# Kernel tuning notes

Measured on AMD Instinct MI355X. Metric: run time of the kernel, lower is better.

Reference implementation:

```python
import jax, jax.numpy as jnp
import numpy as np

N, T1, T2 = 150000, 30000, 8192
E1, E2 = 400000, 160000
F_IN, F_HID, F_OUT = 512, 256, 20


def setup_inputs() -> dict:
    key = jax.random.key(0)
    ks = jax.random.split(key, 10)
    return {
        "x": jax.random.normal(ks[0], (N, F_IN), dtype=jnp.float32),
        "src1": jax.random.randint(ks[1], (E1,), 0, N, dtype=jnp.int32),
        "dst1": jax.random.randint(ks[2], (E1,), 0, T1, dtype=jnp.int32),
        "src2": jax.random.randint(ks[3], (E2,), 0, T1, dtype=jnp.int32),
        "dst2": jax.random.randint(ks[4], (E2,), 0, T2, dtype=jnp.int32),
        "Wl1": jax.random.normal(ks[5], (F_HID, F_IN), dtype=jnp.float32) * 0.05,
        "bl1": jnp.zeros((F_HID,), dtype=jnp.float32),
        "Wr1": jax.random.normal(ks[6], (F_HID, F_IN), dtype=jnp.float32) * 0.05,
        "Wl2": jax.random.normal(ks[7], (F_OUT, F_HID), dtype=jnp.float32) * 0.05,
        "bl2": jnp.zeros((F_OUT,), dtype=jnp.float32),
        "Wr2": jax.random.normal(ks[8], (F_OUT, F_HID), dtype=jnp.float32) * 0.05,
    }


def _sage_conv(x_src, x_tgt, src, dst, num_tgt, Wl, bl, Wr):
    # PyG SAGEConv (mean aggr, root_weight=True, bias on lin_l):
    # out = lin_l(mean_{j in N(i)} x_src[j]) + lin_r(x_tgt[i])
    msg = x_src[src]                                                  # [E, F]
    agg = jax.ops.segment_sum(msg, dst, num_segments=num_tgt)        # [T, F]
    cnt = jax.ops.segment_sum(jnp.ones((src.shape[0],), x_src.dtype), dst,
                              num_segments=num_tgt)                  # [T]
    mean = agg / jnp.maximum(cnt, 1.0)[:, None]
    return mean @ Wl.T + bl + x_tgt @ Wr.T


def reference(x, src1, dst1, src2, dst2, Wl1, bl1, Wr1, Wl2, bl2, Wr2):
    # Layer 1: [N, F_IN] -> [T1, F_HID], relu (eval mode: no dropout)
    h = _sage_conv(x, x[:T1], src1, dst1, T1, Wl1, bl1, Wr1)
    h = jax.nn.relu(h)
    # Layer 2: [T1, F_HID] -> [T2, F_OUT]
    out = _sage_conv(h, h[:T2], src2, dst2, T2, Wl2, bl2, Wr2)
    return jax.nn.log_softmax(out, axis=-1)
```

## Files before the change

kernel.cpp:

```cpp
#include <hip/hip_runtime.h>
#include <math.h>

constexpr int T1N  = 30000;
constexpr int T2N  = 8192;
constexpr int FIN  = 512;
constexpr int FHID = 256;
constexpr int FOUT = 20;

typedef short bf16x8 __attribute__((ext_vector_type(8)));
typedef float f32x4  __attribute__((ext_vector_type(4)));

__device__ __forceinline__ short f2bf(float f) {
    unsigned u = __float_as_uint(f);
    u += 0x7fff + ((u >> 16) & 1);
    return (short)(u >> 16);
}
__device__ __forceinline__ float bf2f(short s) {
    return __uint_as_float(((unsigned)(unsigned short)s) << 16);
}

__device__ __forceinline__ void gload16(const void* g, void* l) {
    __builtin_amdgcn_global_load_lds(
        (const __attribute__((address_space(1))) void*)g,
        (__attribute__((address_space(3))) void*)l, 16, 0, 0);
}

__global__ void count_kernel(const int* __restrict__ dst, int* __restrict__ cnt, int E) {
    int i = blockIdx.x * blockDim.x + threadIdx.x;
    int stride = gridDim.x * blockDim.x;
    for (; i < E; i += stride) atomicAdd(&cnt[dst[i]], 1);
}

__global__ __launch_bounds__(1024) void scan_kernel(const int* __restrict__ cnt,
        int* __restrict__ rs, int* __restrict__ cur, int T) {
    __shared__ int wsum[16];
    int tid = threadIdx.x;
    int lane = tid & 63, wid = tid >> 6;
    int carry = 0;
    for (int base = 0; base < T; base += 4096) {
        int i = base + tid * 4;
        int4 v = make_int4(0, 0, 0, 0);
        if (i + 3 < T) v = *(const int4*)(cnt + i);
        else {
            if (i     < T) v.x = cnt[i];
            if (i + 1 < T) v.y = cnt[i + 1];
            if (i + 2 < T) v.z = cnt[i + 2];
            if (i + 3 < T) v.w = cnt[i + 3];
        }
        int tsum = v.x + v.y + v.z + v.w;
        int s = tsum;
        #pragma unroll
        for (int off = 1; off < 64; off <<= 1) {
            int t = __shfl_up(s, off, 64);
            if (lane >= off) s += t;
        }
        if (lane == 63) wsum[wid] = s;
        __syncthreads();
        if (wid == 0) {
            int w = (lane < 16) ? wsum[lane] : 0;
            #pragma unroll
            for (int off = 1; off < 16; off <<= 1) {
                int t = __shfl_up(w, off, 64);
                if (lane >= off) w += t;
            }
            if (lane < 16) wsum[lane] = w;
        }
        __syncthreads();
        int e0 = s - tsum + (wid > 0 ? wsum[wid - 1] : 0) + carry;
        int e1 = e0 + v.x, e2 = e1 + v.y, e3 = e2 + v.z;
        if (i + 3 < T) {
            *(int4*)(rs + i)  = make_int4(e0, e1, e2, e3);
            *(int4*)(cur + i) = make_int4(e0, e1, e2, e3);
        } else {
            if (i     < T) { rs[i]     = e0; cur[i]     = e0; }
            if (i + 1 < T) { rs[i + 1] = e1; cur[i + 1] = e1; }
            if (i + 2 < T) { rs[i + 2] = e2; cur[i + 2] = e2; }
        }
        int total = wsum[15];
        __syncthreads();
        carry += total;
    }
    if (tid == 0) rs[T] = carry;
}

__global__ void scatter_kernel(const int* __restrict__ src, const int* __restrict__ dst,
        int* __restrict__ cur, int* __restrict__ ss, int E) {
    int i = blockIdx.x * blockDim.x + threadIdx.x;
    int stride = gridDim.x * blockDim.x;
    for (; i < E; i += stride) {
        int d = dst[i];
        int pos = atomicAdd(&cur[d], 1);
        ss[pos] = src[i];
    }
}

__global__ void convert_x_full(const float* __restrict__ x, short* __restrict__ xbf, long n8) {
    long i = ((long)blockIdx.x * blockDim.x + threadIdx.x);
    if (i >= n8) return;
    const float* p = x + i * 8;
    float4 v0 = *(const float4*)p;
    float4 v1 = *(const float4*)(p + 4);
    bf16x8 o;
    o[0] = f2bf(v0.x); o[1] = f2bf(v0.y); o[2] = f2bf(v0.z); o[3] = f2bf(v0.w);
    o[4] = f2bf(v1.x); o[5] = f2bf(v1.y); o[6] = f2bf(v1.z); o[7] = f2bf(v1.w);
    *(bf16x8*)(xbf + i * 8) = o;
}

__global__ void convert_w_kernel(const float* __restrict__ Wl, const float* __restrict__ Wr,
        short* __restrict__ Wcat) {
    int i = (blockIdx.x * blockDim.x + threadIdx.x) * 8;
    if (i >= FHID * 1024) return;
    int n = i >> 10;
    int k = i & 1023;
    const float* sp = (k < 512) ? (Wl + (size_t)n * FIN + k) : (Wr + (size_t)n * FIN + (k - 512));
    float4 v0 = *(const float4*)sp;
    float4 v1 = *(const float4*)(sp + 4);
    bf16x8 o;
    o[0] = f2bf(v0.x); o[1] = f2bf(v0.y); o[2] = f2bf(v0.z); o[3] = f2bf(v0.w);
    o[4] = f2bf(v1.x); o[5] = f2bf(v1.y); o[6] = f2bf(v1.z); o[7] = f2bf(v1.w);
    *(bf16x8*)(Wcat + (size_t)n * 1024 + k) = o;
}

__global__ void agg1_kernel(const short* __restrict__ xbf, const int* __restrict__ ss,
        const int* __restrict__ rs, short* __restrict__ meanbf, int T) {
    int gw = (int)((blockIdx.x * (size_t)blockDim.x + threadIdx.x) >> 6);
    int lane = threadIdx.x & 63;
    if (gw >= T) return;
    int j0 = rs[gw], j1 = rs[gw + 1];
    float a[8] = {};
    for (int j = j0; j < j1; ++j) {
        int s = ss[j];
        bf16x8 v = *(const bf16x8*)(xbf + (size_t)s * FIN + lane * 8);
        #pragma unroll
        for (int q = 0; q < 8; ++q) a[q] += bf2f(v[q]);
    }
    int d = j1 - j0;
    float inv = 1.0f / (float)(d > 1 ? d : 1);
    bf16x8 o;
    #pragma unroll
    for (int q = 0; q < 8; ++q) o[q] = f2bf(a[q] * inv);
    *(bf16x8*)(meanbf + (size_t)gw * FIN + lane * 8) = o;
}

__global__ void agg2_kernel(const float* __restrict__ feat, const int* __restrict__ ss,
        const int* __restrict__ rs, float* __restrict__ mean, int T) {
    int gw = (int)((blockIdx.x * (size_t)blockDim.x + threadIdx.x) >> 6);
    int lane = threadIdx.x & 63;
    if (gw >= T) return;
    int j0 = rs[gw], j1 = rs[gw + 1];
    float4 a = make_float4(0.f, 0.f, 0.f, 0.f);
    for (int j = j0; j < j1; ++j) {
        int s = ss[j];
        float4 v = *(const float4*)(feat + (size_t)s * FHID + lane * 4);
        a.x += v.x; a.y += v.y; a.z += v.z; a.w += v.w;
    }
    int d = j1 - j0;
    float inv = 1.0f / (float)(d > 1 ? d : 1);
    *(float4*)(mean + (size_t)gw * FHID + lane * 4) =
        make_float4(a.x * inv, a.y * inv, a.z * inv, a.w * inv);
}

__global__ __launch_bounds__(256, 2) void gemm1_mfma(
        const short* __restrict__ Am, const short* __restrict__ Ax,
        const short* __restrict__ W, const float* __restrict__ bias,
        float* __restrict__ h) {
    __shared__ short As[2][128 * 32];
    __shared__ short Bs[2][128 * 32];
    int tid = threadIdx.x;
    int wid = tid >> 6, lane = tid & 63;
    int brow = blockIdx.x * 128, bcol = blockIdx.y * 128;
    int wr = (wid >> 1) * 64, wc = (wid & 1) * 64;

    f32x4 acc[4][4] = {};
    int kgrp = lane >> 4;
    int r16 = lane & 15;

    auto stage = [&](int buf, int kt) {
        const short* Abase = (kt < 512) ? Am : Ax;
        int ko = kt & 511;
        #pragma unroll
        for (int c2 = 0; c2 < 2; ++c2) {
            int q = wid + c2 * 4;
            int c = q * 64 + lane;
            int row = c >> 2;
            int rx = (row ^ (row >> 2)) & 3;
            int sl = (c & 3) ^ rx;
            int gr = brow + row; if (gr > T1N - 1) gr = T1N - 1;
            gload16(Abase + (size_t)gr * 512 + ko + sl * 8, (char*)As[buf] + q * 1024);
            gload16(W + (size_t)(bcol + row) * 1024 + kt + sl * 8, (char*)Bs[buf] + q * 1024);
        }
    };

    stage(0, 0);
    __syncthreads();

    int cur = 0;
    for (int kt = 0; kt < 1024; kt += 32) {
        if (kt + 32 < 1024) stage(cur ^ 1, kt + 32);

        bf16x8 af[4], bfr[4];
        #pragma unroll
        for (int m = 0; m < 4; ++m) {
            int row = wr + m * 16 + r16;
            int sl = kgrp ^ ((row ^ (row >> 2)) & 3);
            af[m] = *(const bf16x8*)((const char*)As[cur] + row * 64 + sl * 16);
        }
        #pragma unroll
        for (int n = 0; n < 4; ++n) {
            int row = wc + n * 16 + r16;
            int sl = kgrp ^ ((row ^ (row >> 2)) & 3);
            bfr[n] = *(const bf16x8*)((const char*)Bs[cur] + row * 64 + sl * 16);
        }
        #pragma unroll
        for (int m = 0; m < 4; ++m)
            #pragma unroll
            for (int n = 0; n < 4; ++n)
                acc[m][n] = __builtin_amdgcn_mfma_f32_16x16x32_bf16(
                        af[m], bfr[n], acc[m][n], 0, 0, 0);

        __syncthreads();
        cur ^= 1;
    }

    int g4 = lane >> 4;
    #pragma unroll
    for (int n = 0; n < 4; ++n) {
        int col = bcol + wc + n * 16 + r16;
        float bv = bias[col];
        #pragma unroll
        for (int m = 0; m < 4; ++m) {
            #pragma unroll
            for (int r = 0; r < 4; ++r) {
                int row = brow + wr + m * 16 + g4 * 4 + r;
                if (row < T1N) {
                    float v = acc[m][n][r] + bv;
                    h[(size_t)row * FHID + col] = v > 0.f ? v : 0.f;
                }
            }
        }
    }
}

__global__ __launch_bounds__(256) void gemm2_lsm_kernel(const float* __restrict__ mean2,
        const float* __restrict__ h, const float* __restrict__ Wl,
        const float* __restrict__ Wr, const float* __restrict__ bias,
        float* __restrict__ out) {
    __shared__ float Wls[FOUT * FHID];
    __shared__ float Wrs[FOUT * FHID];
    int tid = threadIdx.x;
    for (int i = tid; i < FOUT * FHID / 4; i += 256) {
        ((float4*)Wls)[i] = ((const float4*)Wl)[i];
        ((float4*)Wrs)[i] = ((const float4*)Wr)[i];
    }
    __syncthreads();

    int row = blockIdx.x * 4 + (tid >> 6);
    int lane = tid & 63;
    if (row >= T2N) return;

    float acc[FOUT];
    #pragma unroll
    for (int o = 0; o < FOUT; ++o) acc[o] = 0.f;

    const float* mrow = mean2 + (size_t)row * FHID;
    const float* hrow = h + (size_t)row * FHID;
    #pragma unroll
    for (int kk = 0; kk < 4; ++kk) {
        int k = lane + kk * 64;
        float m = mrow[k];
        float hr = hrow[k];
        #pragma unroll
        for (int o = 0; o < FOUT; ++o)
            acc[o] = fmaf(m, Wls[o * FHID + k], fmaf(hr, Wrs[o * FHID + k], acc[o]));
    }
    #pragma unroll
    for (int o = 0; o < FOUT; ++o)
        #pragma unroll
        for (int off = 32; off > 0; off >>= 1)
            acc[o] += __shfl_down(acc[o], off, 64);

    if (lane == 0) {
        float mx = -1e30f;
        #pragma unroll
        for (int o = 0; o < FOUT; ++o) {
            acc[o] += bias[o];
            mx = fmaxf(mx, acc[o]);
        }
        float s = 0.f;
        #pragma unroll
        for (int o = 0; o < FOUT; ++o) s += expf(acc[o] - mx);
        float lse = mx + logf(s);
        float* op = out + (size_t)row * FOUT;
        #pragma unroll
        for (int o = 0; o < FOUT; ++o) op[o] = acc[o] - lse;
    }
}

extern "C" void kernel_launch(void* const* d_in, const int* in_sizes, int n_in,
                              void* d_out, int out_size, void* d_ws, size_t ws_size,
                              hipStream_t stream) {
    const float* x   = (const float*)d_in[0];
    const int* src1  = (const int*)d_in[1];
    const int* dst1  = (const int*)d_in[2];
    const int* src2  = (const int*)d_in[3];
    const int* dst2  = (const int*)d_in[4];
    const float* Wl1 = (const float*)d_in[5];
    const float* bl1 = (const float*)d_in[6];
    const float* Wr1 = (const float*)d_in[7];
    const float* Wl2 = (const float*)d_in[8];
    const float* bl2 = (const float*)d_in[9];
    const float* Wr2 = (const float*)d_in[10];
    int E1 = in_sizes[1];
    int E2 = in_sizes[3];
    int N  = in_sizes[0] / FIN;

    char* p = (char*)d_ws;
    auto alloc = [&](size_t bytes) {
        char* r = p;
        p += (bytes + 255) & ~(size_t)255;
        return r;
    };
    short* xbf   = (short*)alloc((size_t)N * FIN * 2);
    short* meanbf= (short*)alloc((size_t)T1N * FIN * 2);
    short* Wcat  = (short*)alloc((size_t)FHID * 1024 * 2);
    float* hbuf  = (float*)alloc((size_t)T1N * FHID * 4);
    float* mean2 = (float*)alloc((size_t)T2N * FHID * 4);
    int* cnt1 = (int*)alloc((size_t)T1N * 4);
    int* cnt2 = (int*)alloc((size_t)T2N * 4);
    int* rs1  = (int*)alloc((size_t)(T1N + 1) * 4);
    int* cur1 = (int*)alloc((size_t)T1N * 4);
    int* ss1  = (int*)alloc((size_t)E1 * 4);
    int* rs2  = (int*)alloc((size_t)(T2N + 1) * 4);
    int* cur2 = (int*)alloc((size_t)T2N * 4);
    int* ss2  = (int*)alloc((size_t)E2 * 4);

    hipMemsetAsync(cnt1, 0, (size_t)((char*)(cnt2 + T2N) - (char*)cnt1), stream);

    count_kernel<<<512, 256, 0, stream>>>(dst1, cnt1, E1);
    count_kernel<<<256, 256, 0, stream>>>(dst2, cnt2, E2);
    scan_kernel<<<1, 1024, 0, stream>>>(cnt1, rs1, cur1, T1N);
    scan_kernel<<<1, 1024, 0, stream>>>(cnt2, rs2, cur2, T2N);
    scatter_kernel<<<512, 256, 0, stream>>>(src1, dst1, cur1, ss1, E1);
    scatter_kernel<<<256, 256, 0, stream>>>(src2, dst2, cur2, ss2, E2);

    convert_w_kernel<<<(FHID * 1024 / 8 + 255) / 256, 256, 0, stream>>>(Wl1, Wr1, Wcat);
    long n8 = (long)N * FIN / 8;
    convert_x_full<<<(int)((n8 + 255) / 256), 256, 0, stream>>>(x, xbf, n8);

    agg1_kernel<<<(T1N * 64 + 255) / 256, 256, 0, stream>>>(xbf, ss1, rs1, meanbf, T1N);
    dim3 g1((T1N + 127) / 128, FHID / 128);
    gemm1_mfma<<<g1, 256, 0, stream>>>(meanbf, xbf, Wcat, bl1, hbuf);

    agg2_kernel<<<(T2N * 64 + 255) / 256, 256, 0, stream>>>(hbuf, ss2, rs2, mean2, T2N);
    gemm2_lsm_kernel<<<T2N / 4, 256, 0, stream>>>(mean2, hbuf, Wl2, Wr2, bl2, (float*)d_out);
}
```

Measured before the change: 685.2 us.

## Reorder both SAGE layers to transform before aggregating and merge graph preprocessing

Layer 1 now projects every source node with Wl1 before gathering, so the gather reads 256-wide bf16 rows instead of 512-wide ones. The root term and ReLU are fused into the aggregation kernel. Layer 2 projects h to a 32-padded width with an MFMA GEMM before aggregating, so its gather is 20-wide, and the final kernel only applies Wr2 plus log-softmax. The count, scan and scatter kernels for the two edge lists are merged into single launches. The cost is a much larger GEMM over all N nodes instead of only T1 targets, plus an extra intermediate buffer to write.

```diff
diff --git a/kernel.cpp b/kernel.cpp
--- a/kernel.cpp
+++ b/kernel.cpp
@@ -6,8 +6,10 @@
 constexpr int FIN  = 512;
 constexpr int FHID = 256;
 constexpr int FOUT = 20;
+constexpr int NPAD = 32;
 
 typedef short bf16x8 __attribute__((ext_vector_type(8)));
+typedef short bf16x4 __attribute__((ext_vector_type(4)));
 typedef float f32x4  __attribute__((ext_vector_type(4)));
 
 __device__ __forceinline__ short f2bf(float f) {
@@ -25,14 +27,24 @@
         (__attribute__((address_space(3))) void*)l, 16, 0, 0);
 }
 
-__global__ void count_kernel(const int* __restrict__ dst, int* __restrict__ cnt, int E) {
+__global__ void count_both(const int* __restrict__ dst1, const int* __restrict__ dst2,
+        int* __restrict__ cnt1, int* __restrict__ cnt2, int E1, int E2) {
     int i = blockIdx.x * blockDim.x + threadIdx.x;
     int stride = gridDim.x * blockDim.x;
-    for (; i < E; i += stride) atomicAdd(&cnt[dst[i]], 1);
-}
-
-__global__ __launch_bounds__(1024) void scan_kernel(const int* __restrict__ cnt,
-        int* __restrict__ rs, int* __restrict__ cur, int T) {
+    int tot = E1 + E2;
+    for (; i < tot; i += stride) {
+        if (i < E1) atomicAdd(&cnt1[dst1[i]], 1);
+        else        atomicAdd(&cnt2[dst2[i - E1]], 1);
+    }
+}
+
+__global__ __launch_bounds__(1024) void scan_both(
+        const int* __restrict__ cnt1, int* __restrict__ rs1, int* __restrict__ cur1,
+        const int* __restrict__ cnt2, int* __restrict__ rs2, int* __restrict__ cur2) {
+    const int* cnt = (blockIdx.x == 0) ? cnt1 : cnt2;
+    int* rs  = (blockIdx.x == 0) ? rs1  : rs2;
+    int* cur = (blockIdx.x == 0) ? cur1 : cur2;
+    int T    = (blockIdx.x == 0) ? T1N  : T2N;
     __shared__ int wsum[16];
     int tid = threadIdx.x;
     int lane = tid & 63, wid = tid >> 6;
@@ -45,7 +57,6 @@
             if (i     < T) v.x = cnt[i];
             if (i + 1 < T) v.y = cnt[i + 1];
             if (i + 2 < T) v.z = cnt[i + 2];
-            if (i + 3 < T) v.w = cnt[i + 3];
         }
         int tsum = v.x + v.y + v.z + v.w;
         int s = tsum;
@@ -83,14 +94,22 @@
     if (tid == 0) rs[T] = carry;
 }
 
-__global__ void scatter_kernel(const int* __restrict__ src, const int* __restrict__ dst,
-        int* __restrict__ cur, int* __restrict__ ss, int E) {
+__global__ void scatter_both(const int* __restrict__ src1, const int* __restrict__ dst1,
+        const int* __restrict__ src2, const int* __restrict__ dst2,
+        int* __restrict__ cur1, int* __restrict__ cur2,
+        int* __restrict__ ss1, int* __restrict__ ss2, int E1, int E2) {
     int i = blockIdx.x * blockDim.x + threadIdx.x;
     int stride = gridDim.x * blockDim.x;
-    for (; i < E; i += stride) {
-        int d = dst[i];
-        int pos = atomicAdd(&cur[d], 1);
-        ss[pos] = src[i];
+    int tot = E1 + E2;
+    for (; i < tot; i += stride) {
+        if (i < E1) {
+            int pos = atomicAdd(&cur1[dst1[i]], 1);
+            ss1[pos] = src1[i];
+        } else {
+            int j = i - E1;
+            int pos = atomicAdd(&cur2[dst2[j]], 1);
+            ss2[pos] = src2[j];
+        }
     }
 }
 
@@ -106,88 +125,183 @@
     *(bf16x8*)(xbf + i * 8) = o;
 }
 
-__global__ void convert_w_kernel(const float* __restrict__ Wl, const float* __restrict__ Wr,
-        short* __restrict__ Wcat) {
+__global__ void convert_w_all(const float* __restrict__ Wl1, const float* __restrict__ Wr1,
+        const float* __restrict__ Wl2, short* __restrict__ Wl1bf,
+        short* __restrict__ Wr1bf, short* __restrict__ Wl2pad) {
     int i = (blockIdx.x * blockDim.x + threadIdx.x) * 8;
-    if (i >= FHID * 1024) return;
-    int n = i >> 10;
-    int k = i & 1023;
-    const float* sp = (k < 512) ? (Wl + (size_t)n * FIN + k) : (Wr + (size_t)n * FIN + (k - 512));
-    float4 v0 = *(const float4*)sp;
-    float4 v1 = *(const float4*)(sp + 4);
-    bf16x8 o;
-    o[0] = f2bf(v0.x); o[1] = f2bf(v0.y); o[2] = f2bf(v0.z); o[3] = f2bf(v0.w);
-    o[4] = f2bf(v1.x); o[5] = f2bf(v1.y); o[6] = f2bf(v1.z); o[7] = f2bf(v1.w);
-    *(bf16x8*)(Wcat + (size_t)n * 1024 + k) = o;
-}
-
-__global__ void agg1_kernel(const short* __restrict__ xbf, const int* __restrict__ ss,
-        const int* __restrict__ rs, short* __restrict__ meanbf, int T) {
+    const int S1 = FHID * FIN;
+    if (i < S1) {
+        const float* sp = Wl1 + i;
+        float4 v0 = *(const float4*)sp, v1 = *(const float4*)(sp + 4);
+        bf16x8 o;
+        o[0]=f2bf(v0.x); o[1]=f2bf(v0.y); o[2]=f2bf(v0.z); o[3]=f2bf(v0.w);
+        o[4]=f2bf(v1.x); o[5]=f2bf(v1.y); o[6]=f2bf(v1.z); o[7]=f2bf(v1.w);
+        *(bf16x8*)(Wl1bf + i) = o;
+    } else if (i < 2 * S1) {
+        const float* sp = Wr1 + (i - S1);
+        float4 v0 = *(const float4*)sp, v1 = *(const float4*)(sp + 4);
+        bf16x8 o;
+        o[0]=f2bf(v0.x); o[1]=f2bf(v0.y); o[2]=f2bf(v0.z); o[3]=f2bf(v0.w);
+        o[4]=f2bf(v1.x); o[5]=f2bf(v1.y); o[6]=f2bf(v1.z); o[7]=f2bf(v1.w);
+        *(bf16x8*)(Wr1bf + (i - S1)) = o;
+    } else if (i < 2 * S1 + NPAD * FHID) {
+        int k = i - 2 * S1;
+        int row = k >> 8;
+        bf16x8 o;
+        if (row < FOUT) {
+            const float* sp = Wl2 + (size_t)row * FHID + (k & 255);
+            float4 v0 = *(const float4*)sp, v1 = *(const float4*)(sp + 4);
+            o[0]=f2bf(v0.x); o[1]=f2bf(v0.y); o[2]=f2bf(v0.z); o[3]=f2bf(v0.w);
+            o[4]=f2bf(v1.x); o[5]=f2bf(v1.y); o[6]=f2bf(v1.z); o[7]=f2bf(v1.w);
+        } else {
+            o = (bf16x8)(short)0;
+        }
+        *(bf16x8*)(Wl2pad + k) = o;
+    }
+}
+
+template <int MODE>
+__global__ __launch_bounds__(256, 2) void gemm_l1(
+        const short* __restrict__ A, const short* __restrict__ W,
+        const float* __restrict__ bias, void* __restrict__ outv, int M) {
+    __shared__ short As[2][128 * 32];
+    __shared__ short Bs[2][256 * 32];
+    int tid = threadIdx.x;
+    int wid = tid >> 6, lane = tid & 63;
+    int brow = blockIdx.x * 128;
+    int wr = (wid >> 1) * 64, wc = (wid & 1) * 128;
+
+    f32x4 acc[4][8] = {};
+    int kgrp = lane >> 4;
+    int r16 = lane & 15;
+
+    auto stage = [&](int buf, int kt) {
+        #pragma unroll
+        for (int c2 = 0; c2 < 2; ++c2) {
+            int q = wid + c2 * 4;
+            int c = q * 64 + lane;
+            int row = c >> 2;
+            int sl = (c & 3) ^ ((row ^ (row >> 2)) & 3);
+            int gr = brow + row; if (gr > M - 1) gr = M - 1;
+            gload16(A + (size_t)gr * 512 + kt + sl * 8, (char*)As[buf] + q * 1024);
+        }
+        #pragma unroll
+        for (int c2 = 0; c2 < 4; ++c2) {
+            int q = wid + c2 * 4;
+            int c = q * 64 + lane;
+            int row = c >> 2;
+            int sl = (c & 3) ^ ((row ^ (row >> 2)) & 3);
+            gload16(W + (size_t)row * 512 + kt + sl * 8, (char*)Bs[buf] + q * 1024);
+        }
+    };
+
+    stage(0, 0);
+    __syncthreads();
+
+    int cur = 0;
+    for (int kt = 0; kt < 512; kt += 32) {
+        if (kt + 32 < 512) stage(cur ^ 1, kt + 32);
+
+        bf16x8 af[4], bfr[8];
+        #pragma unroll
+        for (int m = 0; m < 4; ++m) {
+            int row = wr + m * 16 + r16;
+            int sl = kgrp ^ ((row ^ (row >> 2)) & 3);
+            af[m] = *(const bf16x8*)((const char*)As[cur] + row * 64 + sl * 16);
+        }
+        #pragma unroll
+        for (int n = 0; n < 8; ++n) {
+            int row = wc + n * 16 + r16;
+            int sl = kgrp ^ ((row ^ (row >> 2)) & 3);
+            bfr[n] = *(const bf16x8*)((const char*)Bs[cur] + row * 64 + sl * 16);
+        }
+        #pragma unroll
+        for (int m = 0; m < 4; ++m)
+            #pragma unroll
+            for (int n = 0; n < 8; ++n)
+                acc[m][n] = __builtin_amdgcn_mfma_f32_16x16x32_bf16(
+                        af[m], bfr[n], acc[m][n], 0, 0, 0);
+
+        __syncthreads();
+        cur ^= 1;
+    }
+
+    int g4 = lane >> 4;
+    #pragma unroll
+    for (int n = 0; n < 8; ++n) {
+        int col = wc + n * 16 + r16;
+        float bv = (MODE == 1) ? bias[col] : 0.f;
+        #pragma unroll
+        for (int m = 0; m < 4; ++m) {
+            #pragma unroll
+            for (int r = 0; r < 4; ++r) {
+                int row = brow + wr + m * 16 + g4 * 4 + r;
+                if (row < M) {
+                    if (MODE == 0)
+                        ((short*)outv)[(size_t)row * 256 + col] = f2bf(acc[m][n][r]);
+                    else
+                        ((float*)outv)[(size_t)row * 256 + col] = acc[m][n][r] + bv;
+                }
+            }
+        }
+    }
+}
+
+__global__ void agg1_kernel(const short* __restrict__ y, const int* __restrict__ ss,
+        const int* __restrict__ rs, const float* __restrict__ hr,
+        float* __restrict__ h, short* __restrict__ hbf, int T) {
     int gw = (int)((blockIdx.x * (size_t)blockDim.x + threadIdx.x) >> 6);
     int lane = threadIdx.x & 63;
     if (gw >= T) return;
     int j0 = rs[gw], j1 = rs[gw + 1];
-    float a[8] = {};
+    float a[4] = {};
     for (int j = j0; j < j1; ++j) {
         int s = ss[j];
-        bf16x8 v = *(const bf16x8*)(xbf + (size_t)s * FIN + lane * 8);
-        #pragma unroll
-        for (int q = 0; q < 8; ++q) a[q] += bf2f(v[q]);
+        bf16x4 v = *(const bf16x4*)(y + (size_t)s * FHID + lane * 4);
+        a[0] += bf2f(v[0]); a[1] += bf2f(v[1]); a[2] += bf2f(v[2]); a[3] += bf2f(v[3]);
     }
     int d = j1 - j0;
     float inv = 1.0f / (float)(d > 1 ? d : 1);
-    bf16x8 o;
-    #pragma unroll
-    for (int q = 0; q < 8; ++q) o[q] = f2bf(a[q] * inv);
-    *(bf16x8*)(meanbf + (size_t)gw * FIN + lane * 8) = o;
-}
-
-__global__ void agg2_kernel(const float* __restrict__ feat, const int* __restrict__ ss,
-        const int* __restrict__ rs, float* __restrict__ mean, int T) {
-    int gw = (int)((blockIdx.x * (size_t)blockDim.x + threadIdx.x) >> 6);
-    int lane = threadIdx.x & 63;
-    if (gw >= T) return;
-    int j0 = rs[gw], j1 = rs[gw + 1];
-    float4 a = make_float4(0.f, 0.f, 0.f, 0.f);
-    for (int j = j0; j < j1; ++j) {
-        int s = ss[j];
-        float4 v = *(const float4*)(feat + (size_t)s * FHID + lane * 4);
-        a.x += v.x; a.y += v.y; a.z += v.z; a.w += v.w;
-    }
-    int d = j1 - j0;
-    float inv = 1.0f / (float)(d > 1 ? d : 1);
-    *(float4*)(mean + (size_t)gw * FHID + lane * 4) =
-        make_float4(a.x * inv, a.y * inv, a.z * inv, a.w * inv);
-}
-
-__global__ __launch_bounds__(256, 2) void gemm1_mfma(
-        const short* __restrict__ Am, const short* __restrict__ Ax,
-        const short* __restrict__ W, const float* __restrict__ bias,
-        float* __restrict__ h) {
+    float4 hv = *(const float4*)(hr + (size_t)gw * FHID + lane * 4);
+    float o0 = fmaxf(a[0] * inv + hv.x, 0.f);
+    float o1 = fmaxf(a[1] * inv + hv.y, 0.f);
+    float o2 = fmaxf(a[2] * inv + hv.z, 0.f);
+    float o3 = fmaxf(a[3] * inv + hv.w, 0.f);
+    *(float4*)(h + (size_t)gw * FHID + lane * 4) = make_float4(o0, o1, o2, o3);
+    bf16x4 ob; ob[0] = f2bf(o0); ob[1] = f2bf(o1); ob[2] = f2bf(o2); ob[3] = f2bf(o3);
+    *(bf16x4*)(hbf + (size_t)gw * FHID + lane * 4) = ob;
+}
+
+__global__ __launch_bounds__(128, 2) void gemm_z(
+        const short* __restrict__ A, const short* __restrict__ W,
+        float* __restrict__ z, int M) {
     __shared__ short As[2][128 * 32];
-    __shared__ short Bs[2][128 * 32];
+    __shared__ short Bs[2][32 * 32];
     int tid = threadIdx.x;
     int wid = tid >> 6, lane = tid & 63;
-    int brow = blockIdx.x * 128, bcol = blockIdx.y * 128;
-    int wr = (wid >> 1) * 64, wc = (wid & 1) * 64;
-
-    f32x4 acc[4][4] = {};
+    int brow = blockIdx.x * 128;
+    int wr = wid * 64;
+
+    f32x4 acc[4][2] = {};
     int kgrp = lane >> 4;
     int r16 = lane & 15;
 
     auto stage = [&](int buf, int kt) {
-        const short* Abase = (kt < 512) ? Am : Ax;
-        int ko = kt & 511;
-        #pragma unroll
-        for (int c2 = 0; c2 < 2; ++c2) {
-            int q = wid + c2 * 4;
+        #pragma unroll
+        for (int c2 = 0; c2 < 4; ++c2) {
+            int q = wid + c2 * 2;
             int c = q * 64 + lane;
             int row = c >> 2;
-            int rx = (row ^ (row >> 2)) & 3;
-            int sl = (c & 3) ^ rx;
-            int gr = brow + row; if (gr > T1N - 1) gr = T1N - 1;
-            gload16(Abase + (size_t)gr * 512 + ko + sl * 8, (char*)As[buf] + q * 1024);
-            gload16(W + (size_t)(bcol + row) * 1024 + kt + sl * 8, (char*)Bs[buf] + q * 1024);
+            int sl = (c & 3) ^ ((row ^ (row >> 2)) & 3);
+            int gr = brow + row; if (gr > M - 1) gr = M - 1;
+            gload16(A + (size_t)gr * 256 + kt + sl * 8, (char*)As[buf] + q * 1024);
+        }
+        {
+            int q = wid;
+            int c = q * 64 + lane;
+            int row = c >> 2;
+            int sl = (c & 3) ^ ((row ^ (row >> 2)) & 3);
+            gload16(W + (size_t)row * 256 + kt + sl * 8, (char*)Bs[buf] + q * 1024);
         }
     };
 
@@ -195,10 +309,10 @@
     __syncthreads();
 
     int cur = 0;
-    for (int kt = 0; kt < 1024; kt += 32) {
-        if (kt + 32 < 1024) stage(cur ^ 1, kt + 32);
-
-        bf16x8 af[4], bfr[4];
+    for (int kt = 0; kt < 256; kt += 32) {
+        if (kt + 32 < 256) stage(cur ^ 1, kt + 32);
+
+        bf16x8 af[4], bfr[2];
         #pragma unroll
         for (int m = 0; m < 4; ++m) {
             int row = wr + m * 16 + r16;
@@ -206,15 +320,15 @@
             af[m] = *(const bf16x8*)((const char*)As[cur] + row * 64 + sl * 16);
         }
         #pragma unroll
-        for (int n = 0; n < 4; ++n) {
-            int row = wc + n * 16 + r16;
+        for (int n = 0; n < 2; ++n) {
+            int row = n * 16 + r16;
             int sl = kgrp ^ ((row ^ (row >> 2)) & 3);
             bfr[n] = *(const bf16x8*)((const char*)Bs[cur] + row * 64 + sl * 16);
         }
         #pragma unroll
         for (int m = 0; m < 4; ++m)
             #pragma unroll
-            for (int n = 0; n < 4; ++n)
+            for (int n = 0; n < 2; ++n)
                 acc[m][n] = __builtin_amdgcn_mfma_f32_16x16x32_bf16(
                         af[m], bfr[n], acc[m][n], 0, 0, 0);
 
@@ -224,34 +338,42 @@
 
     int g4 = lane >> 4;
     #pragma unroll
-    for (int n = 0; n < 4; ++n) {
-        int col = bcol + wc + n * 16 + r16;
-        float bv = bias[col];
+    for (int n = 0; n < 2; ++n) {
+        int col = n * 16 + r16;
         #pragma unroll
         for (int m = 0; m < 4; ++m) {
             #pragma unroll
             for (int r = 0; r < 4; ++r) {
                 int row = brow + wr + m * 16 + g4 * 4 + r;
-                if (row < T1N) {
-                    float v = acc[m][n][r] + bv;
-                    h[(size_t)row * FHID + col] = v > 0.f ? v : 0.f;
-                }
+                if (row < M)
+                    z[(size_t)row * NPAD + col] = acc[m][n][r];
             }
         }
     }
 }
 
-__global__ __launch_bounds__(256) void gemm2_lsm_kernel(const float* __restrict__ mean2,
-        const float* __restrict__ h, const float* __restrict__ Wl,
-        const float* __restrict__ Wr, const float* __restrict__ bias,
-        float* __restrict__ out) {
-    __shared__ float Wls[FOUT * FHID];
+__global__ void agg2z_kernel(const float* __restrict__ z, const int* __restrict__ ss,
+        const int* __restrict__ rs, float* __restrict__ mz, int T) {
+    int gw = (int)((blockIdx.x * (size_t)blockDim.x + threadIdx.x) >> 6);
+    int lane = threadIdx.x & 63;
+    int t = gw * 2 + (lane >> 5);
+    int c = lane & 31;
+    if (t >= T) return;
+    int j0 = rs[t], j1 = rs[t + 1];
+    float a = 0.f;
+    for (int j = j0; j < j1; ++j)
+        a += z[(size_t)ss[j] * NPAD + c];
+    int d = j1 - j0;
+    mz[(size_t)t * NPAD + c] = a / (float)(d > 1 ? d : 1);
+}
+
+__global__ __launch_bounds__(256) void lsm_kernel(const float* __restrict__ mz,
+        const float* __restrict__ h, const float* __restrict__ Wr,
+        const float* __restrict__ bias, float* __restrict__ out) {
     __shared__ float Wrs[FOUT * FHID];
     int tid = threadIdx.x;
-    for (int i = tid; i < FOUT * FHID / 4; i += 256) {
-        ((float4*)Wls)[i] = ((const float4*)Wl)[i];
+    for (int i = tid; i < FOUT * FHID / 4; i += 256)
         ((float4*)Wrs)[i] = ((const float4*)Wr)[i];
-    }
     __syncthreads();
 
     int row = blockIdx.x * 4 + (tid >> 6);
@@ -262,16 +384,14 @@
     #pragma unroll
     for (int o = 0; o < FOUT; ++o) acc[o] = 0.f;
 
-    const float* mrow = mean2 + (size_t)row * FHID;
     const float* hrow = h + (size_t)row * FHID;
     #pragma unroll
     for (int kk = 0; kk < 4; ++kk) {
         int k = lane + kk * 64;
-        float m = mrow[k];
-        float hr = hrow[k];
+        float hv = hrow[k];
         #pragma unroll
         for (int o = 0; o < FOUT; ++o)
-            acc[o] = fmaf(m, Wls[o * FHID + k], fmaf(hr, Wrs[o * FHID + k], acc[o]));
+            acc[o] = fmaf(hv, Wrs[o * FHID + k], acc[o]);
     }
     #pragma unroll
     for (int o = 0; o < FOUT; ++o)
@@ -283,7 +403,7 @@
         float mx = -1e30f;
         #pragma unroll
         for (int o = 0; o < FOUT; ++o) {
-            acc[o] += bias[o];
+            acc[o] += mz[(size_t)row * NPAD + o] + bias[o];
             mx = fmaxf(mx, acc[o]);
         }
         float s = 0.f;
@@ -320,11 +440,16 @@
         p += (bytes + 255) & ~(size_t)255;
         return r;
     };
-    short* xbf   = (short*)alloc((size_t)N * FIN * 2);
-    short* meanbf= (short*)alloc((size_t)T1N * FIN * 2);
-    short* Wcat  = (short*)alloc((size_t)FHID * 1024 * 2);
-    float* hbuf  = (float*)alloc((size_t)T1N * FHID * 4);
-    float* mean2 = (float*)alloc((size_t)T2N * FHID * 4);
+    short* xbf    = (short*)alloc((size_t)N * FIN * 2);
+    short* ybuf   = (short*)alloc((size_t)N * FHID * 2);
+    float* hr     = (float*)alloc((size_t)T1N * FHID * 4);
+    float* hbuf   = (float*)alloc((size_t)T1N * FHID * 4);
+    short* hbf    = (short*)alloc((size_t)T1N * FHID * 2);
+    float* zbuf   = (float*)alloc((size_t)T1N * NPAD * 4);
+    float* mz     = (float*)alloc((size_t)T2N * NPAD * 4);
+    short* Wl1bf  = (short*)alloc((size_t)FHID * FIN * 2);
+    short* Wr1bf  = (short*)alloc((size_t)FHID * FIN * 2);
+    short* Wl2pad = (short*)alloc((size_t)NPAD * FHID * 2);
     int* cnt1 = (int*)alloc((size_t)T1N * 4);
     int* cnt2 = (int*)alloc((size_t)T2N * 4);
     int* rs1  = (int*)alloc((size_t)(T1N + 1) * 4);
@@ -336,21 +461,20 @@
 
     hipMemsetAsync(cnt1, 0, (size_t)((char*)(cnt2 + T2N) - (char*)cnt1), stream);
 
-    count_kernel<<<512, 256, 0, stream>>>(dst1, cnt1, E1);
-    count_kernel<<<256, 256, 0, stream>>>(dst2, cnt2, E2);
-    scan_kernel<<<1, 1024, 0, stream>>>(cnt1, rs1, cur1, T1N);
-    scan_kernel<<<1, 1024, 0, stream>>>(cnt2, rs2, cur2, T2N);
-    scatter_kernel<<<512, 256, 0, stream>>>(src1, dst1, cur1, ss1, E1);
-    scatter_kernel<<<256, 256, 0, stream>>>(src2, dst2, cur2, ss2, E2);
-
-    convert_w_kernel<<<(FHID * 1024 / 8 + 255) / 256, 256, 0, stream>>>(Wl1, Wr1, Wcat);
+    count_both<<<768, 256, 0, stream>>>(dst1, dst2, cnt1, cnt2, E1, E2);
+    scan_both<<<2, 1024, 0, stream>>>(cnt1, rs1, cur1, cnt2, rs2, cur2);
+    scatter_both<<<768, 256, 0, stream>>>(src1, dst1, src2, dst2, cur1, cur2, ss1, ss2, E1, E2);
+
+    convert_w_all<<<((2 * FHID * FIN + NPAD * FHID) / 8 + 255) / 256, 256, 0, stream>>>(
+        Wl1, Wr1, Wl2, Wl1bf, Wr1bf, Wl2pad);
     long n8 = (long)N * FIN / 8;
     convert_x_full<<<(int)((n8 + 255) / 256), 256, 0, stream>>>(x, xbf, n8);
 
-    agg1_kernel<<<(T1N * 64 + 255) / 256, 256, 0, stream>>>(xbf, ss1, rs1, meanbf, T1N);
-    dim3 g1((T1N + 127) / 128, FHID / 128);
-    gemm1_mfma<<<g1, 256, 0, stream>>>(meanbf, xbf, Wcat, bl1, hbuf);
-
-    agg2_kernel<<<(T2N * 64 + 255) / 256, 256, 0, stream>>>(hbuf, ss2, rs2, mean2, T2N);
-    gemm2_lsm_kernel<<<T2N / 4, 256, 0, stream>>>(mean2, hbuf, Wl2, Wr2, bl2, (float*)d_out);
-}
+    gemm_l1<1><<<(T1N + 127) / 128, 256, 0, stream>>>(xbf, Wr1bf, bl1, hr, T1N);
+    gemm_l1<0><<<(N + 127) / 128, 256, 0, stream>>>(xbf, Wl1bf, nullptr, ybuf, N);
+    agg1_kernel<<<(T1N * 64 + 255) / 256, 256, 0, stream>>>(ybuf, ss1, rs1, hr, hbuf, hbf, T1N);
+
+    gemm_z<<<(T1N + 127) / 128, 128, 0, stream>>>(hbf, Wl2pad, zbuf, T1N);
+    agg2z_kernel<<<(T2N / 2 * 64 + 255) / 256, 256, 0, stream>>>(zbuf, ss2, rs2, mz, T2N);
+    lsm_kernel<<<T2N / 4, 256, 0, stream>>>(mz, hbuf, Wr2, bl2, (float*)d_out);
+}
```

Result: slower. 728.3 us (+6.3%).
